# Performance work log

Hardware: AMD Instinct MI355X
Metric: run time of the kernel (lower is better)

Reference implementation:

```python
import jax, jax.numpy as jnp
import numpy as np

B, T, H, V = 16, 128, 512, 50257


def setup_inputs() -> dict:
    key = jax.random.key(0)
    ks = jax.random.split(key, 6)
    s = 0.05  # init_scale
    return {
        "tokens": jax.random.randint(ks[0], (B, T), 0, V, dtype=jnp.int32),
        "labels": jax.random.randint(ks[1], (B, T), 0, V, dtype=jnp.int32),
        "embedding": jax.random.normal(ks[2], (V, H), jnp.float32) * s,
        "W1": jax.random.normal(ks[3], (2 * H, 4 * H), jnp.float32) * s,
        "b1": jnp.zeros((4 * H,), jnp.float32),
        "W2": jax.random.normal(ks[4], (2 * H, 4 * H), jnp.float32) * s,
        "b2": jnp.zeros((4 * H,), jnp.float32),
        "softmax_w": jax.random.normal(ks[5], (H, V), jnp.float32) * s,
        "softmax_b": jnp.zeros((V,), jnp.float32),
    }


def _lstm_cell(x, h, c, W, b):
    # TF LSTMCell gate order: i, j (candidate), f, o; forget_bias = 0.0
    z = jnp.concatenate([x, h], axis=-1) @ W + b  # [B, 4H]
    i, j, f, o = jnp.split(z, 4, axis=-1)
    c_new = c * jax.nn.sigmoid(f) + jax.nn.sigmoid(i) * jnp.tanh(j)
    h_new = jnp.tanh(c_new) * jax.nn.sigmoid(o)
    return h_new, c_new


def _forward(tokens, labels, embedding, W1, b1, W2, b2, softmax_w, softmax_b):
    x = embedding[tokens]                 # [B, T, H] embedding lookup
    xs = jnp.swapaxes(x, 0, 1)            # [T, B, H] time-major for scan
    zeros = jnp.zeros((B, H), x.dtype)

    def step(carry, xt):
        c1, h1, c2, h2 = carry
        h1n, c1n = _lstm_cell(xt, h1, c1, W1, b1)
        h2n, c2n = _lstm_cell(h1n, h2, c2, W2, b2)
        return (c1n, h1n, c2n, h2n), h2n

    _, hs = jax.lax.scan(step, (zeros, zeros, zeros, zeros), xs)  # hs: [T, B, H]
    output = jnp.swapaxes(hs, 0, 1).reshape(-1, H)                # [B*T, H]
    logits = output @ softmax_w + softmax_b                       # [B*T, V]
    logp = jax.nn.log_softmax(logits, axis=-1)
    ll = jnp.take_along_axis(logp, labels.reshape(-1, 1), axis=1)[:, 0]
    cost = -jnp.sum(ll) / B  # sequence_loss_by_example summed, / batch_size
    return cost


def reference(tokens, labels, embedding, W1, b1, W2, b2, softmax_w, softmax_b):
    return _forward(tokens, labels, embedding, W1, b1, W2, b2, softmax_w, softmax_b)
```

## Files before the change

### kernel.cpp

```cpp
#include <hip/hip_runtime.h>

#define B_ 16
#define T_ 128
#define H_ 512
#define V_ 50257
#define VP_ 50304
#define NBLK 393
#define M_ (B_*T_)
#define N4H 2048
#define KH 512
#define NKB 16
#define FP_ 32
#define NTILES (NBLK * 16)
#define NWORK 224
#define NCHUNK (VP_ * 16 / 16)
#define HP_ 520

typedef __attribute__((ext_vector_type(8))) short short8;
typedef __attribute__((ext_vector_type(4))) float floatx4;
typedef unsigned long long u64;

static __device__ __forceinline__ unsigned short f2bf(float f) {
    unsigned int u = __builtin_bit_cast(unsigned int, f);
    unsigned int r = (u + 0x7FFFu + ((u >> 16) & 1u)) >> 16;
    return (unsigned short)r;
}
static __device__ __forceinline__ void st_ic(u64* p, u64 v) {
    __hip_atomic_store(p, v, __ATOMIC_RELAXED, __HIP_MEMORY_SCOPE_AGENT);
}

__global__ void k_init(const int* __restrict__ labels, int* __restrict__ lab_r,
                       unsigned short* __restrict__ zeroh, int* __restrict__ flags) {
    int tid = blockIdx.x * blockDim.x + threadIdx.x;
    if (tid < M_) {
        int t = tid >> 4, b = tid & 15;
        lab_r[tid] = labels[b * T_ + t];
    }
    if (tid < B_ * H_) zeroh[tid] = 0;
    if (tid < 34 * FP_) flags[tid] = 0;
}

__global__ void k_embed(const int* __restrict__ tokens, const float* __restrict__ emb,
                        unsigned short* __restrict__ X) {
    int tid = blockIdx.x * blockDim.x + threadIdx.x;
    if (tid >= M_ * H_) return;
    int row = tid >> 9, col = tid & 511;
    int t = row >> 4, b = row & 15;
    int tok = tokens[b * T_ + t];
    X[tid] = f2bf(emb[(size_t)tok * H_ + col]);
}

__global__ void k_pack(const float* __restrict__ src, int ld, int nvalid, int nkb,
                       int nchunks, unsigned short* __restrict__ dst) {
    int tid = blockIdx.x * blockDim.x + threadIdx.x;
    int lane = tid & 63, chunk = tid >> 6;
    if (chunk >= nchunks) return;
    int nt = chunk / nkb, kb = chunk % nkb;
    int n = nt * 16 + (lane & 15);
    int k = kb * 32 + ((lane >> 4) << 3);
    unsigned short vals[8];
    if (n < nvalid) {
#pragma unroll
        for (int j = 0; j < 8; ++j) vals[j] = f2bf(src[(size_t)(k + j) * ld + n]);
    } else {
#pragma unroll
        for (int j = 0; j < 8; ++j) vals[j] = 0;
    }
    *(short8*)(dst + (size_t)chunk * 512 + lane * 8) = *(short8*)vals;
}

__global__ __launch_bounds__(256, 2) void k_gemm_bias(
        const unsigned short* __restrict__ A, const unsigned short* __restrict__ Bp,
        const float* __restrict__ bias, float* __restrict__ C) {
    int bn = blockIdx.x, bm = blockIdx.y;
    int tid = threadIdx.x, lane = tid & 63, w = tid >> 6;
    int wm = w >> 1, wn = w & 1;
    int l15 = lane & 15, quad = lane >> 4;
    floatx4 acc[4][4];
#pragma unroll
    for (int i = 0; i < 4; ++i)
#pragma unroll
        for (int j = 0; j < 4; ++j) acc[i][j] = (floatx4){0.f, 0.f, 0.f, 0.f};
    const unsigned short* Abase = A + (size_t)(bm * 128 + wm * 64 + l15) * KH + quad * 8;
    int ntg0 = bn * 8 + wn * 4;
#pragma unroll 4
    for (int kb = 0; kb < NKB; ++kb) {
        short8 af[4], bf[4];
#pragma unroll
        for (int mt = 0; mt < 4; ++mt) af[mt] = *(const short8*)(Abase + mt * 16 * KH + kb * 32);
#pragma unroll
        for (int nt = 0; nt < 4; ++nt)
            bf[nt] = *(const short8*)(Bp + ((size_t)(ntg0 + nt) * NKB + kb) * 512 + lane * 8);
#pragma unroll
        for (int mt = 0; mt < 4; ++mt)
#pragma unroll
            for (int nt = 0; nt < 4; ++nt)
                acc[mt][nt] = __builtin_amdgcn_mfma_f32_16x16x32_bf16(af[mt], bf[nt], acc[mt][nt], 0, 0, 0);
    }
#pragma unroll
    for (int nt = 0; nt < 4; ++nt) {
        int col = bn * 128 + wn * 64 + nt * 16 + l15;
        float bv = bias[col];
#pragma unroll
        for (int mt = 0; mt < 4; ++mt) {
            int row0 = bm * 128 + wm * 64 + mt * 16 + quad * 4;
#pragma unroll
            for (int r = 0; r < 4; ++r)
                C[(size_t)(row0 + r) * N4H + col] = acc[mt][nt][r] + bv;
        }
    }
}

__global__ __launch_bounds__(512, 2) void k_mega(
        const float* __restrict__ Zpre1, const float* __restrict__ W1,
        const float* __restrict__ W2, const float* __restrict__ b2,
        const unsigned short* __restrict__ zeroh,
        unsigned short* __restrict__ H1, unsigned short* __restrict__ H2,
        int* __restrict__ flags,
        const float* __restrict__ sw, unsigned short* __restrict__ SWP,
        const float* __restrict__ sb, const int* __restrict__ lab_r,
        float* __restrict__ pm, float* __restrict__ ps, float* __restrict__ labv) {
    const int blk = blockIdx.x, tid = threadIdx.x;
    const int lane = tid & 63, w = tid >> 6;
    const int l15 = lane & 15, quad = lane >> 4;
    __shared__ unsigned short hs1[16 * HP_];
    __shared__ unsigned short hs2[16 * HP_];
    __shared__ float zs[128 * 17];
    u64* H1u = (u64*)H1;
    u64* H2u = (u64*)H2;

    if (blk < 32) {
        const bool isL2 = blk >= 16;
        const int bj = isL2 ? blk - 16 : blk;
        const int g = w >> 1, half = w & 1;
        const int nt = g * 32 + bj * 2 + half;
        const int colg = g * 512 + bj * 32 + half * 16 + l15;

        short8 bfr[32];
        {
            unsigned short vals[8];
            if (!isL2) {
#pragma unroll
                for (int kb = 0; kb < 16; ++kb) {
#pragma unroll
                    for (int j = 0; j < 8; ++j)
                        vals[j] = f2bf(W1[(size_t)(512 + kb * 32 + quad * 8 + j) * N4H + nt * 16 + l15]);
                    bfr[kb] = *(short8*)vals;
                }
            } else {
#pragma unroll
                for (int kb = 0; kb < 32; ++kb) {
#pragma unroll
                    for (int j = 0; j < 8; ++j)
                        vals[j] = f2bf(W2[(size_t)(kb * 32 + quad * 8 + j) * N4H + nt * 16 + l15]);
                    bfr[kb] = *(short8*)vals;
                }
            }
        }
        const float b2c = isL2 ? b2[colg] : 0.f;
        float creg = 0.f;

        for (int s = 0; s < T_; ++s) {
            float zpre[4];
            if (!isL2) {
#pragma unroll
                for (int r = 0; r < 4; ++r)
                    zpre[r] = Zpre1[(size_t)(s * 16 + quad * 4 + r) * N4H + colg];
            }
            if (w == 0 && (s > 0 || isL2)) {
                int tgt = 0x80000000;
                int* fp = flags;
                if (!isL2) {
                    if (lane < 16) { fp = flags + lane * FP_; tgt = s; }
                } else {
                    if (lane < 16) { fp = flags + lane * FP_; tgt = s + 1; }
                    else if (lane < 32) { fp = flags + lane * FP_; tgt = s; }
                }
                bool act = (!isL2 && lane < 16) || (isL2 && lane < 32);
                while (true) {
                    int v = act ? __hip_atomic_load(fp, __ATOMIC_RELAXED, __HIP_MEMORY_SCOPE_AGENT)
                                : 0x7fffffff;
                    if (__all(v >= tgt)) break;
                    __builtin_amdgcn_s_sleep(1);
                }
            }
            __syncthreads();

            if (!isL2) {
                const short8* src = (const short8*)((s == 0) ? zeroh
                                       : H1 + (size_t)(s - 1) * B_ * H_);
#pragma unroll
                for (int j = 0; j < 2; ++j) {
                    int idx = j * 512 + tid;
                    short8 v = src[idx];
                    *(short8*)(&hs1[(idx >> 6) * HP_ + (idx & 63) * 8]) = v;
                }
            } else {
                const short8* s1 = (const short8*)(H1 + (size_t)s * B_ * H_);
                const short8* s2 = (const short8*)((s == 0) ? zeroh
                                       : H2 + (size_t)(s - 1) * B_ * H_);
#pragma unroll
                for (int j = 0; j < 2; ++j) {
                    int idx = j * 512 + tid;
                    short8 v = s1[idx];
                    *(short8*)(&hs1[(idx >> 6) * HP_ + (idx & 63) * 8]) = v;
                }
#pragma unroll
                for (int j = 0; j < 2; ++j) {
                    int idx = j * 512 + tid;
                    short8 v = s2[idx];
                    *(short8*)(&hs2[(idx >> 6) * HP_ + (idx & 63) * 8]) = v;
                }
            }
            __syncthreads();

            if (!isL2) {
                floatx4 a0 = (floatx4){0.f,0.f,0.f,0.f}, a1 = (floatx4){0.f,0.f,0.f,0.f};
#pragma unroll
                for (int kb = 0; kb < 8; ++kb) {
                    short8 af = *(const short8*)(&hs1[l15 * HP_ + kb * 32 + quad * 8]);
                    a0 = __builtin_amdgcn_mfma_f32_16x16x32_bf16(af, bfr[kb], a0, 0, 0, 0);
                }
#pragma unroll
                for (int kb = 8; kb < 16; ++kb) {
                    short8 af = *(const short8*)(&hs1[l15 * HP_ + kb * 32 + quad * 8]);
                    a1 = __builtin_amdgcn_mfma_f32_16x16x32_bf16(af, bfr[kb], a1, 0, 0, 0);
                }
                const int zcol = g * 32 + half * 16 + l15;
#pragma unroll
                for (int r = 0; r < 4; ++r)
                    zs[zcol * 17 + quad * 4 + r] = a0[r] + a1[r] + zpre[r];
            } else {
                floatx4 a0 = (floatx4){0.f,0.f,0.f,0.f}, a1 = (floatx4){0.f,0.f,0.f,0.f};
#pragma unroll
                for (int kb = 0; kb < 16; ++kb) {
                    short8 af = *(const short8*)(&hs1[l15 * HP_ + kb * 32 + quad * 8]);
                    a0 = __builtin_amdgcn_mfma_f32_16x16x32_bf16(af, bfr[kb], a0, 0, 0, 0);
                }
#pragma unroll
                for (int kb = 0; kb < 16; ++kb) {
                    short8 af = *(const short8*)(&hs2[l15 * HP_ + kb * 32 + quad * 8]);
                    a1 = __builtin_amdgcn_mfma_f32_16x16x32_bf16(af, bfr[16 + kb], a1, 0, 0, 0);
                }
                const int zcol = g * 32 + half * 16 + l15;
#pragma unroll
                for (int r = 0; r < 4; ++r)
                    zs[zcol * 17 + quad * 4 + r] = a0[r] + a1[r] + b2c;
            }
            __syncthreads();

            {
                int u = tid >> 4, b = tid & 15;
                float zi = zs[(0 * 32 + u) * 17 + b];
                float zj = zs[(1 * 32 + u) * 17 + b];
                float zf = zs[(2 * 32 + u) * 17 + b];
                float zo = zs[(3 * 32 + u) * 17 + b];
                float si = 1.f / (1.f + __expf(-zi));
                float sf = 1.f / (1.f + __expf(-zf));
                float so = 1.f / (1.f + __expf(-zo));
                float cn = creg * sf + si * tanhf(zj);
                creg = cn;
                int hvi = (int)f2bf(tanhf(cn) * so);
                int lb = lane & 15;
                unsigned int h0 = (unsigned int)__shfl(hvi, lb);
                unsigned int h1v = (unsigned int)__shfl(hvi, lb + 16);
                unsigned int h2v = (unsigned int)__shfl(hvi, lb + 32);
                unsigned int h3v = (unsigned int)__shfl(hvi, lb + 48);
                if (lane < 16) {
                    u64 v = (u64)(h0 | (h1v << 16)) | ((u64)(h2v | (h3v << 16)) << 32);
                    u64* Hd = isL2 ? H2u : H1u;
                    st_ic(Hd + (size_t)(s * 16 + lane) * 128 + bj * 8 + w, v);
                }
            }
            __builtin_amdgcn_s_waitcnt(0x0F70);
            __syncthreads();
            if (tid == 0)
                __hip_atomic_store(flags + blk * FP_, s + 1, __ATOMIC_RELAXED,
                                   __HIP_MEMORY_SCOPE_AGENT);
        }
    } else {
        const int wid = blk - 32;
        int* wdone = flags + 32 * FP_;

        for (int t = 0; ; ++t) {
            int c = wid + NWORK * (8 * t + w);
            if (c >= NCHUNK) break;
            int cnt = c >> 4, ckb = c & 15;
            int n = cnt * 16 + l15;
            int kk = ckb * 32 + quad * 8;
            unsigned short vals[8];
            if (n < V_) {
#pragma unroll
                for (int j = 0; j < 8; ++j) vals[j] = f2bf(sw[(size_t)(kk + j) * V_ + n]);
            } else {
#pragma unroll
                for (int j = 0; j < 8; ++j) vals[j] = 0;
            }
            u64 v0 = (u64)vals[0] | ((u64)vals[1] << 16) | ((u64)vals[2] << 32) | ((u64)vals[3] << 48);
            u64 v1 = (u64)vals[4] | ((u64)vals[5] << 16) | ((u64)vals[6] << 32) | ((u64)vals[7] << 48);
            u64* dst = (u64*)(SWP + (size_t)c * 512 + lane * 8);
            st_ic(dst, v0);
            st_ic(dst + 1, v1);
        }
        __builtin_amdgcn_s_waitcnt(0x0F70);
        __syncthreads();
        if (tid == 0)
            __hip_atomic_fetch_add(wdone, 1, __ATOMIC_RELAXED, __HIP_MEMORY_SCOPE_AGENT);
        if (w == 0) {
            while (true) {
                int v = (lane == 0)
                    ? __hip_atomic_load(wdone, __ATOMIC_RELAXED, __HIP_MEMORY_SCOPE_AGENT)
                    : 0x7fffffff;
                if (__all(v >= NWORK)) break;
                __builtin_amdgcn_s_sleep(8);
            }
        }
        __syncthreads();

        int done_seen = 0;
        for (int k = wid; k < NTILES; k += NWORK) {
            int bm = k / NBLK, bn = k - bm * NBLK;
            int tgt = bm * 8 + 8;
            if (tgt > done_seen) {
                if (w == 0) {
                    int* fp = flags + (16 + (lane & 15)) * FP_;
                    while (true) {
                        int v = (lane < 16)
                            ? __hip_atomic_load(fp, __ATOMIC_RELAXED, __HIP_MEMORY_SCOPE_AGENT)
                            : 0x7fffffff;
                        if (__all(v >= tgt)) break;
                        __builtin_amdgcn_s_sleep(8);
                    }
                }
                __syncthreads();
                done_seen = tgt;
            }
            floatx4 acc[8];
#pragma unroll
            for (int j = 0; j < 8; ++j) acc[j] = (floatx4){0.f, 0.f, 0.f, 0.f};
            const short8* Abase = (const short8*)(H2 + (size_t)(bm * 128 + w * 16 + l15) * KH) + quad;
            int ntg0 = bn * 8;
#pragma unroll 4
            for (int kb = 0; kb < NKB; ++kb) {
                short8 af = Abase[kb * 4];
#pragma unroll
                for (int nt = 0; nt < 8; ++nt) {
                    short8 bf = *(const short8*)(SWP + ((size_t)(ntg0 + nt) * NKB + kb) * 512 + lane * 8);
                    acc[nt] = __builtin_amdgcn_mfma_f32_16x16x32_bf16(af, bf, acc[nt], 0, 0, 0);
                }
            }
            float bv[8]; int colg[8]; bool valid[8];
#pragma unroll
            for (int nt = 0; nt < 8; ++nt) {
                colg[nt] = bn * 128 + nt * 16 + l15;
                valid[nt] = colg[nt] < V_;
                bv[nt] = valid[nt] ? sb[colg[nt]] : 0.f;
            }
#pragma unroll
            for (int r = 0; r < 4; ++r) {
                float m = -3.0e38f;
#pragma unroll
                for (int nt = 0; nt < 8; ++nt) {
                    float v = valid[nt] ? acc[nt][r] + bv[nt] : -3.0e38f;
                    acc[nt][r] = v;
                    m = fmaxf(m, v);
                }
#pragma unroll
                for (int d = 1; d < 16; d <<= 1) m = fmaxf(m, __shfl_xor(m, d, 16));
                float sm = 0.f;
#pragma unroll
                for (int nt = 0; nt < 8; ++nt)
                    if (valid[nt]) sm += __expf(acc[nt][r] - m);
#pragma unroll
                for (int d = 1; d < 16; d <<= 1) sm += __shfl_xor(sm, d, 16);
                int rowg = bm * 128 + w * 16 + quad * 4 + r;
                int lc = lab_r[rowg];
#pragma unroll
                for (int nt = 0; nt < 8; ++nt)
                    if (valid[nt] && colg[nt] == lc) labv[rowg] = acc[nt][r];
                if (l15 == 0) {
                    pm[(size_t)rowg * NBLK + bn] = m;
                    ps[(size_t)rowg * NBLK + bn] = sm;
                }
            }
        }
    }
}

__global__ void k_rowreduce(const float* __restrict__ pm, const float* __restrict__ ps,
                            const float* __restrict__ labv, float* __restrict__ ll) {
    int row = blockIdx.x;
    int lane = threadIdx.x;
    const float* pmr = pm + (size_t)row * NBLK;
    const float* psr = ps + (size_t)row * NBLK;
    float m = -3.0e38f;
    for (int j = lane; j < NBLK; j += 64) m = fmaxf(m, pmr[j]);
#pragma unroll
    for (int d = 1; d < 64; d <<= 1) m = fmaxf(m, __shfl_xor(m, d, 64));
    float s = 0.f;
    for (int j = lane; j < NBLK; j += 64) s += psr[j] * __expf(pmr[j] - m);
#pragma unroll
    for (int d = 1; d < 64; d <<= 1) s += __shfl_xor(s, d, 64);
    if (lane == 0) ll[row] = labv[row] - m - logf(s);
}

__global__ void k_final(const float* __restrict__ ll, float* __restrict__ out) {
    int lane = threadIdx.x;
    float s = 0.f;
    for (int i = lane; i < M_; i += 64) s += ll[i];
#pragma unroll
    for (int d = 1; d < 64; d <<= 1) s += __shfl_xor(s, d, 64);
    if (lane == 0) out[0] = -s / (float)B_;
}

extern "C" void kernel_launch(void* const* d_in, const int* in_sizes, int n_in,
                              void* d_out, int out_size, void* d_ws, size_t ws_size,
                              hipStream_t stream) {
    const int* tokens = (const int*)d_in[0];
    const int* labels = (const int*)d_in[1];
    const float* emb = (const float*)d_in[2];
    const float* W1 = (const float*)d_in[3];
    const float* b1 = (const float*)d_in[4];
    const float* W2 = (const float*)d_in[5];
    const float* b2 = (const float*)d_in[6];
    const float* sw = (const float*)d_in[7];
    const float* sb = (const float*)d_in[8];
    float* out = (float*)d_out;

    char* ws = (char*)d_ws;
    size_t off = 0;
    auto alloc = [&](size_t bytes) {
        void* p = ws + off;
        off = (off + bytes + 255) & ~(size_t)255;
        return p;
    };
    unsigned short* X    = (unsigned short*)alloc((size_t)M_ * KH * 2);
    unsigned short* H1   = (unsigned short*)alloc((size_t)M_ * KH * 2);
    unsigned short* H2   = (unsigned short*)alloc((size_t)M_ * KH * 2);
    unsigned short* W1xP = (unsigned short*)alloc((size_t)N4H * KH * 2);
    unsigned short* SWP  = (unsigned short*)alloc((size_t)VP_ * KH * 2);
    float* Z     = (float*)alloc((size_t)M_ * N4H * 4);
    unsigned short* zeroh = (unsigned short*)alloc((size_t)B_ * H_ * 2);
    float* pm   = (float*)alloc((size_t)M_ * NBLK * 4);
    float* ps   = (float*)alloc((size_t)M_ * NBLK * 4);
    float* labv = (float*)alloc((size_t)M_ * 4);
    int*   lab_r = (int*)alloc((size_t)M_ * 4);
    float* ll   = (float*)alloc((size_t)M_ * 4);
    int*   flags = (int*)alloc((size_t)34 * FP_ * 4);

    k_init<<<64, 256, 0, stream>>>(labels, lab_r, zeroh, flags);
    k_embed<<<(M_ * H_) / 256, 256, 0, stream>>>(tokens, emb, X);
    k_pack<<<512, 256, 0, stream>>>(W1, N4H, N4H, 16, 2048, W1xP);

    k_gemm_bias<<<dim3(16, 16), 256, 0, stream>>>(X, W1xP, b1, Z);

    k_mega<<<256, 512, 0, stream>>>(Z, W1, W2, b2, zeroh, H1, H2, flags,
                                    sw, SWP, sb, lab_r, pm, ps, labv);

    k_rowreduce<<<M_, 64, 0, stream>>>(pm, ps, labv, ll);
    k_final<<<1, 64, 0, stream>>>(ll, out);
}
```

Baseline: 765.0 us.

## Split LSTM layer loops, overlap layer-2 recurrent matmul, pair vocab tiles per block

Layer 1 and layer 2 recurrent blocks now run separate loops. Layer 2 computes the h2 (recurrent) half of its matmul before waiting for layer 1's h at step s, which takes one input off the critical dependency chain. The spin-wait sleeps are removed on the recurrent path and lengthened in the vocab workers. Vocab GEMM workers now process two tiles per iteration, with each wave computing two 16-row sub-tiles that share each B fragment load. This halves B traffic per tile but doubles accumulator registers and may lower occupancy.

```diff
diff --git a/kernel.cpp b/kernel.cpp
--- a/kernel.cpp
+++ b/kernel.cpp
@@ -12,6 +12,7 @@
 #define NKB 16
 #define FP_ 32
 #define NTILES (NBLK * 16)
+#define NPAIR (NTILES / 2)
 #define NWORK 224
 #define NCHUNK (VP_ * 16 / 16)
 #define HP_ 520
@@ -160,61 +161,33 @@
         const float b2c = isL2 ? b2[colg] : 0.f;
         float creg = 0.f;
 
-        for (int s = 0; s < T_; ++s) {
-            float zpre[4];
-            if (!isL2) {
+        if (!isL2) {
+            for (int s = 0; s < T_; ++s) {
+                float zpre[4];
 #pragma unroll
                 for (int r = 0; r < 4; ++r)
                     zpre[r] = Zpre1[(size_t)(s * 16 + quad * 4 + r) * N4H + colg];
-            }
-            if (w == 0 && (s > 0 || isL2)) {
-                int tgt = 0x80000000;
-                int* fp = flags;
-                if (!isL2) {
-                    if (lane < 16) { fp = flags + lane * FP_; tgt = s; }
-                } else {
-                    if (lane < 16) { fp = flags + lane * FP_; tgt = s + 1; }
-                    else if (lane < 32) { fp = flags + lane * FP_; tgt = s; }
-                }
-                bool act = (!isL2 && lane < 16) || (isL2 && lane < 32);
-                while (true) {
-                    int v = act ? __hip_atomic_load(fp, __ATOMIC_RELAXED, __HIP_MEMORY_SCOPE_AGENT)
-                                : 0x7fffffff;
-                    if (__all(v >= tgt)) break;
-                    __builtin_amdgcn_s_sleep(1);
-                }
-            }
-            __syncthreads();
-
-            if (!isL2) {
-                const short8* src = (const short8*)((s == 0) ? zeroh
-                                       : H1 + (size_t)(s - 1) * B_ * H_);
-#pragma unroll
-                for (int j = 0; j < 2; ++j) {
-                    int idx = j * 512 + tid;
-                    short8 v = src[idx];
-                    *(short8*)(&hs1[(idx >> 6) * HP_ + (idx & 63) * 8]) = v;
-                }
-            } else {
-                const short8* s1 = (const short8*)(H1 + (size_t)s * B_ * H_);
-                const short8* s2 = (const short8*)((s == 0) ? zeroh
-                                       : H2 + (size_t)(s - 1) * B_ * H_);
-#pragma unroll
-                for (int j = 0; j < 2; ++j) {
-                    int idx = j * 512 + tid;
-                    short8 v = s1[idx];
-                    *(short8*)(&hs1[(idx >> 6) * HP_ + (idx & 63) * 8]) = v;
-                }
-#pragma unroll
-                for (int j = 0; j < 2; ++j) {
-                    int idx = j * 512 + tid;
-                    short8 v = s2[idx];
-                    *(short8*)(&hs2[(idx >> 6) * HP_ + (idx & 63) * 8]) = v;
-                }
-            }
-            __syncthreads();
-
-            if (!isL2) {
+                if (w == 0 && s > 0) {
+                    int* fp = flags + (lane & 15) * FP_;
+                    while (true) {
+                        int v = (lane < 16)
+                            ? __hip_atomic_load(fp, __ATOMIC_RELAXED, __HIP_MEMORY_SCOPE_AGENT)
+                            : 0x7fffffff;
+                        if (__all(v >= s)) break;
+                    }
+                }
+                __syncthreads();
+                {
+                    const short8* src = (const short8*)((s == 0) ? zeroh
+                                           : H1 + (size_t)(s - 1) * B_ * H_);
+#pragma unroll
+                    for (int j = 0; j < 2; ++j) {
+                        int idx = j * 512 + tid;
+                        short8 v = src[idx];
+                        *(short8*)(&hs1[(idx >> 6) * HP_ + (idx & 63) * 8]) = v;
+                    }
+                }
+                __syncthreads();
                 floatx4 a0 = (floatx4){0.f,0.f,0.f,0.f}, a1 = (floatx4){0.f,0.f,0.f,0.f};
 #pragma unroll
                 for (int kb = 0; kb < 8; ++kb) {
@@ -230,57 +203,129 @@
 #pragma unroll
                 for (int r = 0; r < 4; ++r)
                     zs[zcol * 17 + quad * 4 + r] = a0[r] + a1[r] + zpre[r];
-            } else {
-                floatx4 a0 = (floatx4){0.f,0.f,0.f,0.f}, a1 = (floatx4){0.f,0.f,0.f,0.f};
+                __syncthreads();
+                {
+                    int u = tid >> 4, b = tid & 15;
+                    float zi = zs[(0 * 32 + u) * 17 + b];
+                    float zj = zs[(1 * 32 + u) * 17 + b];
+                    float zf = zs[(2 * 32 + u) * 17 + b];
+                    float zo = zs[(3 * 32 + u) * 17 + b];
+                    float si = 1.f / (1.f + __expf(-zi));
+                    float sf = 1.f / (1.f + __expf(-zf));
+                    float so = 1.f / (1.f + __expf(-zo));
+                    float cn = creg * sf + si * tanhf(zj);
+                    creg = cn;
+                    int hvi = (int)f2bf(tanhf(cn) * so);
+                    int lb = lane & 15;
+                    unsigned int h0 = (unsigned int)__shfl(hvi, lb);
+                    unsigned int h1v = (unsigned int)__shfl(hvi, lb + 16);
+                    unsigned int h2v = (unsigned int)__shfl(hvi, lb + 32);
+                    unsigned int h3v = (unsigned int)__shfl(hvi, lb + 48);
+                    if (lane < 16) {
+                        u64 v = (u64)(h0 | (h1v << 16)) | ((u64)(h2v | (h3v << 16)) << 32);
+                        st_ic(H1u + (size_t)(s * 16 + lane) * 128 + bj * 8 + w, v);
+                    }
+                }
+                __builtin_amdgcn_s_waitcnt(0x0F70);
+                __syncthreads();
+                if (tid == 0)
+                    __hip_atomic_store(flags + blk * FP_, s + 1, __ATOMIC_RELAXED,
+                                       __HIP_MEMORY_SCOPE_AGENT);
+            }
+        } else {
+            for (int s = 0; s < T_; ++s) {
+                if (w == 0 && s > 0) {
+                    int* fp = flags + (16 + (lane & 15)) * FP_;
+                    while (true) {
+                        int v = (lane < 16)
+                            ? __hip_atomic_load(fp, __ATOMIC_RELAXED, __HIP_MEMORY_SCOPE_AGENT)
+                            : 0x7fffffff;
+                        if (__all(v >= s)) break;
+                    }
+                }
+                __syncthreads();
+                {
+                    const short8* s2 = (const short8*)((s == 0) ? zeroh
+                                           : H2 + (size_t)(s - 1) * B_ * H_);
+#pragma unroll
+                    for (int j = 0; j < 2; ++j) {
+                        int idx = j * 512 + tid;
+                        short8 v = s2[idx];
+                        *(short8*)(&hs2[(idx >> 6) * HP_ + (idx & 63) * 8]) = v;
+                    }
+                }
+                __syncthreads();
+                floatx4 a1 = (floatx4){0.f,0.f,0.f,0.f};
+#pragma unroll
+                for (int kb = 0; kb < 16; ++kb) {
+                    short8 af = *(const short8*)(&hs2[l15 * HP_ + kb * 32 + quad * 8]);
+                    a1 = __builtin_amdgcn_mfma_f32_16x16x32_bf16(af, bfr[16 + kb], a1, 0, 0, 0);
+                }
+                if (w == 0) {
+                    int* fp = flags + (lane & 15) * FP_;
+                    while (true) {
+                        int v = (lane < 16)
+                            ? __hip_atomic_load(fp, __ATOMIC_RELAXED, __HIP_MEMORY_SCOPE_AGENT)
+                            : 0x7fffffff;
+                        if (__all(v >= s + 1)) break;
+                    }
+                }
+                __syncthreads();
+                {
+                    const short8* s1 = (const short8*)(H1 + (size_t)s * B_ * H_);
+#pragma unroll
+                    for (int j = 0; j < 2; ++j) {
+                        int idx = j * 512 + tid;
+                        short8 v = s1[idx];
+                        *(short8*)(&hs1[(idx >> 6) * HP_ + (idx & 63) * 8]) = v;
+                    }
+                }
+                __syncthreads();
+                floatx4 a0 = (floatx4){0.f,0.f,0.f,0.f};
 #pragma unroll
                 for (int kb = 0; kb < 16; ++kb) {
                     short8 af = *(const short8*)(&hs1[l15 * HP_ + kb * 32 + quad * 8]);
                     a0 = __builtin_amdgcn_mfma_f32_16x16x32_bf16(af, bfr[kb], a0, 0, 0, 0);
                 }
-#pragma unroll
-                for (int kb = 0; kb < 16; ++kb) {
-                    short8 af = *(const short8*)(&hs2[l15 * HP_ + kb * 32 + quad * 8]);
-                    a1 = __builtin_amdgcn_mfma_f32_16x16x32_bf16(af, bfr[16 + kb], a1, 0, 0, 0);
-                }
                 const int zcol = g * 32 + half * 16 + l15;
 #pragma unroll
                 for (int r = 0; r < 4; ++r)
                     zs[zcol * 17 + quad * 4 + r] = a0[r] + a1[r] + b2c;
-            }
-            __syncthreads();
-
-            {
-                int u = tid >> 4, b = tid & 15;
-                float zi = zs[(0 * 32 + u) * 17 + b];
-                float zj = zs[(1 * 32 + u) * 17 + b];
-                float zf = zs[(2 * 32 + u) * 17 + b];
-                float zo = zs[(3 * 32 + u) * 17 + b];
-                float si = 1.f / (1.f + __expf(-zi));
-                float sf = 1.f / (1.f + __expf(-zf));
-                float so = 1.f / (1.f + __expf(-zo));
-                float cn = creg * sf + si * tanhf(zj);
-                creg = cn;
-                int hvi = (int)f2bf(tanhf(cn) * so);
-                int lb = lane & 15;
-                unsigned int h0 = (unsigned int)__shfl(hvi, lb);
-                unsigned int h1v = (unsigned int)__shfl(hvi, lb + 16);
-                unsigned int h2v = (unsigned int)__shfl(hvi, lb + 32);
-                unsigned int h3v = (unsigned int)__shfl(hvi, lb + 48);
-                if (lane < 16) {
-                    u64 v = (u64)(h0 | (h1v << 16)) | ((u64)(h2v | (h3v << 16)) << 32);
-                    u64* Hd = isL2 ? H2u : H1u;
-                    st_ic(Hd + (size_t)(s * 16 + lane) * 128 + bj * 8 + w, v);
-                }
-            }
-            __builtin_amdgcn_s_waitcnt(0x0F70);
-            __syncthreads();
-            if (tid == 0)
-                __hip_atomic_store(flags + blk * FP_, s + 1, __ATOMIC_RELAXED,
-                                   __HIP_MEMORY_SCOPE_AGENT);
+                __syncthreads();
+                {
+                    int u = tid >> 4, b = tid & 15;
+                    float zi = zs[(0 * 32 + u) * 17 + b];
+                    float zj = zs[(1 * 32 + u) * 17 + b];
+                    float zf = zs[(2 * 32 + u) * 17 + b];
+                    float zo = zs[(3 * 32 + u) * 17 + b];
+                    float si = 1.f / (1.f + __expf(-zi));
+                    float sf = 1.f / (1.f + __expf(-zf));
+                    float so = 1.f / (1.f + __expf(-zo));
+                    float cn = creg * sf + si * tanhf(zj);
+                    creg = cn;
+                    int hvi = (int)f2bf(tanhf(cn) * so);
+                    int lb = lane & 15;
+                    unsigned int h0 = (unsigned int)__shfl(hvi, lb);
+                    unsigned int h1v = (unsigned int)__shfl(hvi, lb + 16);
+                    unsigned int h2v = (unsigned int)__shfl(hvi, lb + 32);
+                    unsigned int h3v = (unsigned int)__shfl(hvi, lb + 48);
+                    if (lane < 16) {
+                        u64 v = (u64)(h0 | (h1v << 16)) | ((u64)(h2v | (h3v << 16)) << 32);
+                        st_ic(H2u + (size_t)(s * 16 + lane) * 128 + bj * 8 + w, v);
+                    }
+                }
+                __builtin_amdgcn_s_waitcnt(0x0F70);
+                __syncthreads();
+                if (tid == 0)
+                    __hip_atomic_store(flags + blk * FP_, s + 1, __ATOMIC_RELAXED,
+                                       __HIP_MEMORY_SCOPE_AGENT);
+            }
         }
     } else {
         const int wid = blk - 32;
         int* wdone = flags + 32 * FP_;
+        const int grp = w >> 2;
+        const int wig = w & 3;
 
         for (int t = 0; ; ++t) {
             int c = wid + NWORK * (8 * t + w);
@@ -312,15 +357,17 @@
                     ? __hip_atomic_load(wdone, __ATOMIC_RELAXED, __HIP_MEMORY_SCOPE_AGENT)
                     : 0x7fffffff;
                 if (__all(v >= NWORK)) break;
-                __builtin_amdgcn_s_sleep(8);
+                __builtin_amdgcn_s_sleep(32);
             }
         }
         __syncthreads();
 
         int done_seen = 0;
-        for (int k = wid; k < NTILES; k += NWORK) {
-            int bm = k / NBLK, bn = k - bm * NBLK;
-            int tgt = bm * 8 + 8;
+        for (int p = wid; p < NPAIR; p += NWORK) {
+            int t0 = 2 * p, t1 = 2 * p + 1;
+            int bm0 = t0 / NBLK, bm1 = t1 / NBLK;
+            int bmx = bm0 > bm1 ? bm0 : bm1;
+            int tgt = bmx * 8 + 8;
             if (tgt > done_seen) {
                 if (w == 0) {
                     int* fp = flags + (16 + (lane & 15)) * FP_;
@@ -329,24 +376,31 @@
                             ? __hip_atomic_load(fp, __ATOMIC_RELAXED, __HIP_MEMORY_SCOPE_AGENT)
                             : 0x7fffffff;
                         if (__all(v >= tgt)) break;
-                        __builtin_amdgcn_s_sleep(8);
+                        __builtin_amdgcn_s_sleep(32);
                     }
                 }
                 __syncthreads();
                 done_seen = tgt;
             }
-            floatx4 acc[8];
-#pragma unroll
-            for (int j = 0; j < 8; ++j) acc[j] = (floatx4){0.f, 0.f, 0.f, 0.f};
-            const short8* Abase = (const short8*)(H2 + (size_t)(bm * 128 + w * 16 + l15) * KH) + quad;
+            const int myt = grp ? t1 : t0;
+            const int bm = myt / NBLK, bn = myt - bm * NBLK;
+            floatx4 acc[2][8];
+#pragma unroll
+            for (int st = 0; st < 2; ++st)
+#pragma unroll
+                for (int j = 0; j < 8; ++j) acc[st][j] = (floatx4){0.f, 0.f, 0.f, 0.f};
+            const short8* A0 = (const short8*)(H2 + (size_t)(bm * 128 + wig * 16 + l15) * KH) + quad;
+            const short8* A1 = (const short8*)(H2 + (size_t)(bm * 128 + (wig + 4) * 16 + l15) * KH) + quad;
             int ntg0 = bn * 8;
 #pragma unroll 4
             for (int kb = 0; kb < NKB; ++kb) {
-                short8 af = Abase[kb * 4];
+                short8 af0 = A0[kb * 4];
+                short8 af1 = A1[kb * 4];
 #pragma unroll
                 for (int nt = 0; nt < 8; ++nt) {
                     short8 bf = *(const short8*)(SWP + ((size_t)(ntg0 + nt) * NKB + kb) * 512 + lane * 8);
-                    acc[nt] = __builtin_amdgcn_mfma_f32_16x16x32_bf16(af, bf, acc[nt], 0, 0, 0);
+                    acc[0][nt] = __builtin_amdgcn_mfma_f32_16x16x32_bf16(af0, bf, acc[0][nt], 0, 0, 0);
+                    acc[1][nt] = __builtin_amdgcn_mfma_f32_16x16x32_bf16(af1, bf, acc[1][nt], 0, 0, 0);
                 }
             }
             float bv[8]; int colg[8]; bool valid[8];
@@ -357,30 +411,33 @@
                 bv[nt] = valid[nt] ? sb[colg[nt]] : 0.f;
             }
 #pragma unroll
-            for (int r = 0; r < 4; ++r) {
-                float m = -3.0e38f;
-#pragma unroll
-                for (int nt = 0; nt < 8; ++nt) {
-                    float v = valid[nt] ? acc[nt][r] + bv[nt] : -3.0e38f;
-                    acc[nt][r] = v;
-                    m = fmaxf(m, v);
-                }
-#pragma unroll
-                for (int d = 1; d < 16; d <<= 1) m = fmaxf(m, __shfl_xor(m, d, 16));
-                float sm = 0.f;
-#pragma unroll
-                for (int nt = 0; nt < 8; ++nt)
-                    if (valid[nt]) sm += __expf(acc[nt][r] - m);
-#pragma unroll
-                for (int d = 1; d < 16; d <<= 1) sm += __shfl_xor(sm, d, 16);
-                int rowg = bm * 128 + w * 16 + quad * 4 + r;
-                int lc = lab_r[rowg];
-#pragma unroll
-                for (int nt = 0; nt < 8; ++nt)
-                    if (valid[nt] && colg[nt] == lc) labv[rowg] = acc[nt][r];
-                if (l15 == 0) {
-                    pm[(size_t)rowg * NBLK + bn] = m;
-                    ps[(size_t)rowg * NBLK + bn] = sm;
+            for (int st = 0; st < 2; ++st) {
+#pragma unroll
+                for (int r = 0; r < 4; ++r) {
+                    float m = -3.0e38f;
+#pragma unroll
+                    for (int nt = 0; nt < 8; ++nt) {
+                        float v = valid[nt] ? acc[st][nt][r] + bv[nt] : -3.0e38f;
+                        acc[st][nt][r] = v;
+                        m = fmaxf(m, v);
+                    }
+#pragma unroll
+                    for (int d = 1; d < 16; d <<= 1) m = fmaxf(m, __shfl_xor(m, d, 16));
+                    float sm = 0.f;
+#pragma unroll
+                    for (int nt = 0; nt < 8; ++nt)
+                        if (valid[nt]) sm += __expf(acc[st][nt][r] - m);
+#pragma unroll
+                    for (int d = 1; d < 16; d <<= 1) sm += __shfl_xor(sm, d, 16);
+                    int rowg = bm * 128 + (wig + st * 4) * 16 + quad * 4 + r;
+                    int lc = lab_r[rowg];
+#pragma unroll
+                    for (int nt = 0; nt < 8; ++nt)
+                        if (valid[nt] && colg[nt] == lc) labv[rowg] = acc[st][nt][r];
+                    if (l15 == 0) {
+                        pm[(size_t)rowg * NBLK + bn] = m;
+                        ps[(size_t)rowg * NBLK + bn] = sm;
+                    }
                 }
             }
         }
```

Result: slower. 819.6 us (+7.1%).
